# Performance work log

Measured on AMD Instinct MI355X. Metric: run time of the kernel, lower is better.

## Reference

```python
import jax, jax.numpy as jnp
import numpy as np

D_ENC = 512
D_DEC = 512
D_JOINT = D_ENC + D_DEC  # 1024
V = 1024


def setup_inputs() -> dict:
    key = jax.random.key(0)
    ks = jax.random.split(key, 8)
    s = lambda fan_in: 1.0 / np.sqrt(fan_in)
    return {
        "encoder_output": jax.random.normal(ks[0], (8, 200, D_ENC), dtype=jnp.float32),
        "decoder_output": jax.random.normal(ks[1], (8, 50, D_DEC), dtype=jnp.float32),
        "W_enc": jax.random.uniform(ks[2], (D_JOINT, D_ENC), jnp.float32, -s(D_ENC), s(D_ENC)),
        "b_enc": jax.random.uniform(ks[3], (D_JOINT,), jnp.float32, -s(D_ENC), s(D_ENC)),
        "W_dec": jax.random.uniform(ks[4], (D_JOINT, D_DEC), jnp.float32, -s(D_DEC), s(D_DEC)),
        "b_dec": jax.random.uniform(ks[5], (D_JOINT,), jnp.float32, -s(D_DEC), s(D_DEC)),
        "W_fc": jax.random.uniform(ks[6], (V, D_JOINT), jnp.float32, -s(D_JOINT), s(D_JOINT)),
        "b_fc": jax.random.uniform(ks[7], (V,), jnp.float32, -s(D_JOINT), s(D_JOINT)),
    }


def reference(encoder_output, decoder_output, W_enc, b_enc, W_dec, b_dec, W_fc, b_fc):
    # enc: (B, T, D_JOINT); dec: (B, U, D_JOINT)
    enc = jnp.einsum('btd,jd->btj', encoder_output, W_enc) + b_enc
    dec = jnp.einsum('bud,jd->buj', decoder_output, W_dec) + b_dec
    # broadcast join: (B, T, U, D_JOINT)
    combined = enc[:, :, None, :] + dec[:, None, :, :]
    logits = jnp.einsum('btuj,vj->btuv', jnp.tanh(combined), W_fc) + b_fc
    return jax.nn.log_softmax(logits, axis=-1)
```

## Files before the change

kernel.cpp:

```cpp
#include <hip/hip_runtime.h>
#include <hip/hip_bf16.h>
#include <hip/hip_fp8.h>

#define TT 200
#define UU 50
#define BB 8
#define DJ 1024
#define DE 512
#define VV 1024
#define M_TOTAL (BB*TT*UU)
#define MB 80
#define NITER 32
#define WINV (1.0f/32.0f)

typedef float f32x4 __attribute__((ext_vector_type(4)));

__device__ __forceinline__ float fast_tanh(float x) {
    float e = __expf(2.f * x);
    return 1.f - 2.f / (e + 1.f);
}

__device__ __forceinline__ unsigned char f2fp8(float x) {
    return __hip_fp8_e4m3(x).__x;
}

__device__ __forceinline__ unsigned long long tanh_pack_fp8(float4 e0, float4 e1, float4 d0, float4 d1) {
    unsigned long long r;
    r  = (unsigned long long)f2fp8(fast_tanh(e0.x + d0.x));
    r |= (unsigned long long)f2fp8(fast_tanh(e0.y + d0.y)) << 8;
    r |= (unsigned long long)f2fp8(fast_tanh(e0.z + d0.z)) << 16;
    r |= (unsigned long long)f2fp8(fast_tanh(e0.w + d0.w)) << 24;
    r |= (unsigned long long)f2fp8(fast_tanh(e1.x + d1.x)) << 32;
    r |= (unsigned long long)f2fp8(fast_tanh(e1.y + d1.y)) << 40;
    r |= (unsigned long long)f2fp8(fast_tanh(e1.z + d1.z)) << 48;
    r |= (unsigned long long)f2fp8(fast_tanh(e1.w + d1.w)) << 56;
    return r;
}

__device__ __forceinline__ void gload_lds16(const unsigned char* g, unsigned char* l) {
    __builtin_amdgcn_global_load_lds(
        (const __attribute__((address_space(1))) unsigned int*)(const void*)g,
        (__attribute__((address_space(3))) unsigned int*)(void*)l, 16, 0, 0);
}

__global__ void k_wfct(const float* __restrict__ w, unsigned char* __restrict__ o) {
    const int G = blockIdx.x * 256 + threadIdx.x;
    const int gk = G >> 10, n = G & 1023;
    const float* src = w + (size_t)n * DJ + gk * 8;
    float4 a = *(const float4*)(src);
    float4 b = *(const float4*)(src + 4);
    unsigned long long r;
    r  = (unsigned long long)f2fp8(a.x * 32.f);
    r |= (unsigned long long)f2fp8(a.y * 32.f) << 8;
    r |= (unsigned long long)f2fp8(a.z * 32.f) << 16;
    r |= (unsigned long long)f2fp8(a.w * 32.f) << 24;
    r |= (unsigned long long)f2fp8(b.x * 32.f) << 32;
    r |= (unsigned long long)f2fp8(b.y * 32.f) << 40;
    r |= (unsigned long long)f2fp8(b.z * 32.f) << 48;
    r |= (unsigned long long)f2fp8(b.w * 32.f) << 56;
    *(unsigned long long*)(o + (size_t)G * 8) = r;
}

__global__ __launch_bounds__(256) void k_proj2(const float* __restrict__ enc,
                                               const float* __restrict__ dec,
                                               const float* __restrict__ W_enc,
                                               const float* __restrict__ b_enc,
                                               const float* __restrict__ W_dec,
                                               const float* __restrict__ b_dec,
                                               float* __restrict__ encp,
                                               float* __restrict__ decp) {
    __shared__ float in_s[16][DE];
    const bool isDec = blockIdx.x >= 100;
    const float* in  = isDec ? dec   : enc;
    const float* W   = isDec ? W_dec : W_enc;
    const float* bia = isDec ? b_dec : b_enc;
    float* out       = isDec ? decp  : encp;
    const int NR     = isDec ? (BB*UU) : (BB*TT);
    const int m0 = (isDec ? (blockIdx.x - 100) : blockIdx.x) * 16;
    const int tid = threadIdx.x;
    #pragma unroll
    for (int it = 0; it < 8; ++it) {
        int idx = tid + it * 256;
        int r = idx >> 7, c = (idx & 127) << 2;
        *(float4*)&in_s[r][c] = *(const float4*)(in + (size_t)(m0 + r) * DE + c);
    }
    __syncthreads();
    const int j = blockIdx.y * 256 + tid;
    const float4* wr = (const float4*)(W + (size_t)j * DE);
    float acc[16];
    #pragma unroll
    for (int r = 0; r < 16; ++r) acc[r] = 0.f;
    for (int d4 = 0; d4 < DE / 4; ++d4) {
        float4 w = wr[d4];
        #pragma unroll
        for (int r = 0; r < 16; ++r) {
            float4 x = *(const float4*)&in_s[r][d4 << 2];
            acc[r] += x.x * w.x + x.y * w.y + x.z * w.z + x.w * w.w;
        }
    }
    float bv = bia[j];
    const int gk = j >> 3, kl = j & 7;
    #pragma unroll
    for (int r = 0; r < 16; ++r)
        out[((size_t)gk * NR + (m0 + r)) * 8 + kl] = acc[r] + bv;
}

__global__ __launch_bounds__(512, 2) void k_joint(const float* __restrict__ encp,
                                                  const float* __restrict__ decp,
                                                  const unsigned char* __restrict__ wfc8,
                                                  const float* __restrict__ bfc,
                                                  float* __restrict__ out) {
    __shared__ unsigned char As[81920];
    __shared__ unsigned char Bs[2][32768];
    __shared__ float red[8][MB];

    const int tid = threadIdx.x;
    const int wave = tid >> 6, lane = tid & 63;
    const int g = lane >> 4, ln = lane & 15;
    const int bid = blockIdx.x;
    const int m0 = bid * MB;

    {
        const unsigned char* s0 = wfc8 + (size_t)(bid & 31) * 32768;
        #pragma unroll
        for (int r = 0; r < 4; ++r)
            gload_lds16(s0 + (r * 512 + tid) * 16, &Bs[0][(r * 512 + tid) * 16]);
    }
    for (int r = 0; r < 20; ++r) {
        const int gidx = r * 512 + tid;
        const int gkf = gidx / MB;
        const int m = gidx - gkf * MB;
        const int mrow = m0 + m;
        const int b = mrow / (TT * UU);
        const int rem = mrow - b * (TT * UU);
        const int t = rem / UU;
        const int u = rem - t * UU;
        const float* ep = encp + ((size_t)gkf * (BB * TT) + b * TT + t) * 8;
        const float* dp = decp + ((size_t)gkf * (BB * UU) + b * UU + u) * 8;
        float4 e0 = *(const float4*)(ep);
        float4 e1 = *(const float4*)(ep + 4);
        float4 d0 = *(const float4*)(dp);
        float4 d1 = *(const float4*)(dp + 4);
        *(unsigned long long*)&As[(size_t)gidx * 8] = tanh_pack_fp8(e0, e1, d0, d1);
    }

    f32x4 acc[5][8];
    #pragma unroll
    for (int mf = 0; mf < 5; ++mf)
        #pragma unroll
        for (int nf = 0; nf < 8; ++nf)
            acc[mf][nf] = (f32x4){0.f, 0.f, 0.f, 0.f};

    for (int t = 0; t < NITER; ++t) {
        const int cur = t & 1, nxt = cur ^ 1;
        const int kb = (t + bid) & 31;
        const unsigned char* srcN = wfc8 + (size_t)((t + 1 + bid) & 31) * 32768;
        if (t < NITER - 1) {
            gload_lds16(srcN + (size_t)tid * 16, &Bs[nxt][(size_t)tid * 16]);
            asm volatile("s_waitcnt vmcnt(1) lgkmcnt(0)" ::: "memory");
        } else {
            asm volatile("s_waitcnt vmcnt(0) lgkmcnt(0)" ::: "memory");
        }
        __builtin_amdgcn_sched_barrier(0);
        __builtin_amdgcn_s_barrier();

        long afr[5];
        #pragma unroll
        for (int ph = 0; ph < 4; ++ph) {
            if (ph == 0) {
                #pragma unroll
                for (int mf = 0; mf < 5; ++mf)
                    afr[mf] = *(const long*)&As[(size_t)((kb * 4 + g) * MB + mf * 16 + ln) * 8];
            }
            long bfr[2];
            #pragma unroll
            for (int q = 0; q < 2; ++q)
                bfr[q] = *(const long*)&Bs[cur][(size_t)(g * 1024 + wave * 128 + (ph * 2 + q) * 16 + ln) * 8];
            if (t < NITER - 1 && ph < 3)
                gload_lds16(srcN + (size_t)((ph + 1) * 512 + tid) * 16,
                            &Bs[nxt][(size_t)((ph + 1) * 512 + tid) * 16]);
            __builtin_amdgcn_sched_barrier(0);
            __builtin_amdgcn_s_barrier();
            asm volatile("s_waitcnt lgkmcnt(0)" ::: "memory");
            __builtin_amdgcn_sched_barrier(0);
            __builtin_amdgcn_s_setprio(1);
            #pragma unroll
            for (int q = 0; q < 2; ++q)
                #pragma unroll
                for (int mf = 0; mf < 5; ++mf)
                    acc[mf][ph * 2 + q] = __builtin_amdgcn_mfma_f32_16x16x32_fp8_fp8(afr[mf], bfr[q], acc[mf][ph * 2 + q], 0, 0, 0);
            __builtin_amdgcn_s_setprio(0);
            __builtin_amdgcn_sched_barrier(0);
            __builtin_amdgcn_s_barrier();
        }
    }

    float bv[8];
    #pragma unroll
    for (int nf = 0; nf < 8; ++nf) bv[nf] = bfc[wave * 128 + nf * 16 + ln];
    #pragma unroll
    for (int mf = 0; mf < 5; ++mf)
        #pragma unroll
        for (int nf = 0; nf < 8; ++nf)
            #pragma unroll
            for (int j = 0; j < 4; ++j)
                acc[mf][nf][j] = acc[mf][nf][j] * WINV + bv[nf];

    float rmx[5][4];
    #pragma unroll
    for (int mf = 0; mf < 5; ++mf)
        #pragma unroll
        for (int j = 0; j < 4; ++j) {
            float mx = -3.0e38f;
            #pragma unroll
            for (int nf = 0; nf < 8; ++nf) mx = fmaxf(mx, acc[mf][nf][j]);
            #pragma unroll
            for (int s = 1; s < 16; s <<= 1) mx = fmaxf(mx, __shfl_xor(mx, s));
            rmx[mf][j] = mx;
        }
    if (ln == 0) {
        #pragma unroll
        for (int mf = 0; mf < 5; ++mf)
            #pragma unroll
            for (int j = 0; j < 4; ++j)
                red[wave][mf * 16 + g * 4 + j] = rmx[mf][j];
    }
    __syncthreads();
    #pragma unroll
    for (int mf = 0; mf < 5; ++mf)
        #pragma unroll
        for (int j = 0; j < 4; ++j) {
            const int r = mf * 16 + g * 4 + j;
            float mx = red[0][r];
            #pragma unroll
            for (int w = 1; w < 8; ++w) mx = fmaxf(mx, red[w][r]);
            rmx[mf][j] = mx;
        }
    __syncthreads();

    float rsm[5][4];
    #pragma unroll
    for (int mf = 0; mf < 5; ++mf)
        #pragma unroll
        for (int j = 0; j < 4; ++j) {
            float s = 0.f;
            #pragma unroll
            for (int nf = 0; nf < 8; ++nf) s += __expf(acc[mf][nf][j] - rmx[mf][j]);
            #pragma unroll
            for (int t2 = 1; t2 < 16; t2 <<= 1) s += __shfl_xor(s, t2);
            rsm[mf][j] = s;
        }
    if (ln == 0) {
        #pragma unroll
        for (int mf = 0; mf < 5; ++mf)
            #pragma unroll
            for (int j = 0; j < 4; ++j)
                red[wave][mf * 16 + g * 4 + j] = rsm[mf][j];
    }
    __syncthreads();
    #pragma unroll
    for (int mf = 0; mf < 5; ++mf)
        #pragma unroll
        for (int j = 0; j < 4; ++j) {
            const int r = mf * 16 + g * 4 + j;
            float s = 0.f;
            #pragma unroll
            for (int w = 0; w < 8; ++w) s += red[w][r];
            const float lse = rmx[mf][j] + __logf(s);
            float* op = out + (size_t)(m0 + r) * VV + wave * 128 + ln;
            #pragma unroll
            for (int nf = 0; nf < 8; ++nf)
                __builtin_nontemporal_store(acc[mf][nf][j] - lse, op + nf * 16);
        }
}

extern "C" void kernel_launch(void* const* d_in, const int* in_sizes, int n_in,
                              void* d_out, int out_size, void* d_ws, size_t ws_size,
                              hipStream_t stream) {
    const float* enc   = (const float*)d_in[0];
    const float* dec   = (const float*)d_in[1];
    const float* W_enc = (const float*)d_in[2];
    const float* b_enc = (const float*)d_in[3];
    const float* W_dec = (const float*)d_in[4];
    const float* b_dec = (const float*)d_in[5];
    const float* W_fc  = (const float*)d_in[6];
    const float* b_fc  = (const float*)d_in[7];
    float* out = (float*)d_out;

    float* encp = (float*)d_ws;
    float* decp = encp + (size_t)BB * TT * DJ;
    unsigned char* wfc8 = (unsigned char*)(decp + (size_t)BB * UU * DJ);

    k_wfct<<<(VV * DJ) / (256 * 8), 256, 0, stream>>>(W_fc, wfc8);
    k_proj2<<<dim3(125, DJ / 256), 256, 0, stream>>>(enc, dec, W_enc, b_enc, W_dec, b_dec, encp, decp);
    k_joint<<<M_TOTAL / MB, 512, 0, stream>>>(encp, decp, wfc8, b_fc, out);
}
```

Before: 373.8 us.

## Load FP8 W_fc fragments directly from global memory instead of LDS double-buffering

```diff
diff --git a/kernel.cpp b/kernel.cpp
--- a/kernel.cpp
+++ b/kernel.cpp
@@ -35,12 +35,6 @@
     r |= (unsigned long long)f2fp8(fast_tanh(e1.z + d1.z)) << 48;
     r |= (unsigned long long)f2fp8(fast_tanh(e1.w + d1.w)) << 56;
     return r;
-}
-
-__device__ __forceinline__ void gload_lds16(const unsigned char* g, unsigned char* l) {
-    __builtin_amdgcn_global_load_lds(
-        (const __attribute__((address_space(1))) unsigned int*)(const void*)g,
-        (__attribute__((address_space(3))) unsigned int*)(void*)l, 16, 0, 0);
 }
 
 __global__ void k_wfct(const float* __restrict__ w, unsigned char* __restrict__ o) {
@@ -111,7 +105,6 @@
                                                   const float* __restrict__ bfc,
                                                   float* __restrict__ out) {
     __shared__ unsigned char As[81920];
-    __shared__ unsigned char Bs[2][32768];
     __shared__ float red[8][MB];
 
     const int tid = threadIdx.x;
@@ -120,12 +113,6 @@
     const int bid = blockIdx.x;
     const int m0 = bid * MB;
 
-    {
-        const unsigned char* s0 = wfc8 + (size_t)(bid & 31) * 32768;
-        #pragma unroll
-        for (int r = 0; r < 4; ++r)
-            gload_lds16(s0 + (r * 512 + tid) * 16, &Bs[0][(r * 512 + tid) * 16]);
-    }
     for (int r = 0; r < 20; ++r) {
         const int gidx = r * 512 + tid;
         const int gkf = gidx / MB;
@@ -151,47 +138,23 @@
         for (int nf = 0; nf < 8; ++nf)
             acc[mf][nf] = (f32x4){0.f, 0.f, 0.f, 0.f};
 
+    __syncthreads();
+
+    const unsigned char* bbase = wfc8 + (size_t)(wave * 128 + ln) * 8;
+
     for (int t = 0; t < NITER; ++t) {
-        const int cur = t & 1, nxt = cur ^ 1;
         const int kb = (t + bid) & 31;
-        const unsigned char* srcN = wfc8 + (size_t)((t + 1 + bid) & 31) * 32768;
-        if (t < NITER - 1) {
-            gload_lds16(srcN + (size_t)tid * 16, &Bs[nxt][(size_t)tid * 16]);
-            asm volatile("s_waitcnt vmcnt(1) lgkmcnt(0)" ::: "memory");
-        } else {
-            asm volatile("s_waitcnt vmcnt(0) lgkmcnt(0)" ::: "memory");
-        }
-        __builtin_amdgcn_sched_barrier(0);
-        __builtin_amdgcn_s_barrier();
-
         long afr[5];
         #pragma unroll
-        for (int ph = 0; ph < 4; ++ph) {
-            if (ph == 0) {
-                #pragma unroll
-                for (int mf = 0; mf < 5; ++mf)
-                    afr[mf] = *(const long*)&As[(size_t)((kb * 4 + g) * MB + mf * 16 + ln) * 8];
-            }
-            long bfr[2];
-            #pragma unroll
-            for (int q = 0; q < 2; ++q)
-                bfr[q] = *(const long*)&Bs[cur][(size_t)(g * 1024 + wave * 128 + (ph * 2 + q) * 16 + ln) * 8];
-            if (t < NITER - 1 && ph < 3)
-                gload_lds16(srcN + (size_t)((ph + 1) * 512 + tid) * 16,
-                            &Bs[nxt][(size_t)((ph + 1) * 512 + tid) * 16]);
-            __builtin_amdgcn_sched_barrier(0);
-            __builtin_amdgcn_s_barrier();
-            asm volatile("s_waitcnt lgkmcnt(0)" ::: "memory");
-            __builtin_amdgcn_sched_barrier(0);
-            __builtin_amdgcn_s_setprio(1);
-            #pragma unroll
-            for (int q = 0; q < 2; ++q)
-                #pragma unroll
-                for (int mf = 0; mf < 5; ++mf)
-                    acc[mf][ph * 2 + q] = __builtin_amdgcn_mfma_f32_16x16x32_fp8_fp8(afr[mf], bfr[q], acc[mf][ph * 2 + q], 0, 0, 0);
-            __builtin_amdgcn_s_setprio(0);
-            __builtin_amdgcn_sched_barrier(0);
-            __builtin_amdgcn_s_barrier();
+        for (int mf = 0; mf < 5; ++mf)
+            afr[mf] = *(const long*)&As[(size_t)((kb * 4 + g) * MB + mf * 16 + ln) * 8];
+        const unsigned char* bchunk = bbase + (size_t)(kb * 4 + g) * 1024 * 8;
+        #pragma unroll
+        for (int nf = 0; nf < 8; ++nf) {
+            long bfr = *(const long*)(bchunk + (size_t)nf * 16 * 8);
+            #pragma unroll
+            for (int mf = 0; mf < 5; ++mf)
+                acc[mf][nf] = __builtin_amdgcn_mfma_f32_16x16x32_fp8_fp8(afr[mf], bfr, acc[mf][nf], 0, 0, 0);
         }
     }
 
```

New measurement: 325.7 us. 1.15x faster.
